# Optimization experiments

Measured on AMD Instinct MI355X. Metric: run time of the kernel, lower is better.

## Reference

```python
import jax, jax.numpy as jnp
import numpy as np

N, D, G, C, M = 4096, 256, 4, 10, 5  # nodes, feat dim, batches, centroids, clusterings


def setup_inputs() -> dict:
    key = jax.random.key(0)
    k1, k2, k3, k4 = jax.random.split(key, 4)
    adj = jax.random.uniform(k1, (N, N), dtype=jnp.float32)
    enc_rep = jax.random.normal(k2, (N, D), dtype=jnp.float32)
    batch_id = jax.random.randint(k3, (N,), 0, G, dtype=jnp.int32)
    cluster_labels = jax.random.randint(k4, (M, N), 0, C, dtype=jnp.int32)
    return {"adj": adj, "enc_rep": enc_rep, "batch_id": batch_id,
            "cluster_labels": cluster_labels, "top_k": 20, "top_k_inter": 10}


def reference(adj, enc_rep, batch_id, cluster_labels, top_k, top_k_inter):
    n = enc_rep.shape[0]
    NEG = jnp.float32(-1e30)
    rows = jnp.arange(n)

    # 'similarity' metric: raw inner-product similarity, full N x N once
    sim = enc_rep @ enc_rep.T                                # [N, N]
    same = batch_id[:, None] == batch_id[None, :]            # same-batch mask

    # intra: top_k+1 within own batch group, drop first (self) column
    intra_sim = jnp.where(same, sim, NEG)
    _, intra_idx = jax.lax.top_k(intra_sim, top_k + 1)
    intra_idx = intra_idx[:, 1:]                              # [N, top_k]

    # inter: top_k_inter among all other batch groups
    inter_sim = jnp.where(same, NEG, sim)
    _, inter_idx = jax.lax.top_k(inter_sim, top_k_inter)      # [N, top_k_inter]

    knn_idx = jnp.concatenate([intra_idx, inter_idx], axis=1)  # [N, k_tot]

    # rep_adj[j, i] = 1 iff j is a knn of i  (coo rows=neighbors, cols=node)
    B = jnp.zeros((n, n), jnp.float32).at[knn_idx, rows[:, None]].set(1.0)
    # common_adj = rep_adj * (rep_adj.T > 0), diag zeroed (mutual-knn graph)
    common = B * B.T
    common = common.at[rows, rows].set(0.0)

    # locality = knn_neighbor * adj
    locality = common * adj

    # padded-neighbor validity mask (I_knn_padded != -1 analog): mutual neighbors
    mutual = common[rows[:, None], knn_idx] > 0               # [N, k_tot]

    # per-clustering close-neighbor test, combined across clusterings
    nb_lbl = cluster_labels[:, knn_idx]                       # [M, N, k_tot]
    eq = cluster_labels[:, :, None] == nb_lbl                 # [M, N, k_tot]
    curr = eq | mutual[None]                                  # curr_close_nei = eq | bool_mask
    all_close = jnp.all(curr, axis=0)                         # AND across clusterings

    return locality, all_close.astype(jnp.float32)
```

## Files before the change

### kernel.cpp

```cpp
#include <hip/hip_runtime.h>
#include <hip/hip_bf16.h>
#include <cfloat>

#define NN 4096
#define DD 256
#define MM 5
#define K_TOT 30
#define TGT_INTRA 32
#define TGT_INTER 24
#define CAND_CAP 64

typedef __attribute__((ext_vector_type(8))) short bf16x8;
typedef __attribute__((ext_vector_type(4))) float f32x4;

__device__ __forceinline__ void async16(const void* g, void* l) {
    __builtin_amdgcn_global_load_lds((__attribute__((address_space(1))) void*)g,
                                     (__attribute__((address_space(3))) void*)l,
                                     16, 0, 0);
}

__global__ __launch_bounds__(256) void convert_bf16(const float* __restrict__ E,
                                                    ushort* __restrict__ Eb) {
    const int idx = blockIdx.x * 256 + threadIdx.x;
    const float4 f = ((const float4*)E)[idx];
    ushort4 h;
    {
        __hip_bfloat16 a = __float2bfloat16(f.x); h.x = *(ushort*)&a;
        __hip_bfloat16 b = __float2bfloat16(f.y); h.y = *(ushort*)&b;
        __hip_bfloat16 c = __float2bfloat16(f.z); h.z = *(ushort*)&c;
        __hip_bfloat16 d = __float2bfloat16(f.w); h.w = *(ushort*)&d;
    }
    ((ushort4*)Eb)[idx] = h;
}

__global__ __launch_bounds__(256) void gemm_bf16(const ushort* __restrict__ Eb,
                                                 ushort* __restrict__ simb) {
    __shared__ union {
        struct { ushort A[128 * 32]; ushort B[128 * 32]; } s;
        ushort stage[32 * 136];
    } lds;

    const int t = threadIdx.x;
    const int w = t >> 6, lane = t & 63;
    const int quad = lane >> 4, mr = lane & 15;
    const int rowBase = blockIdx.y * 128, colBase = blockIdx.x * 128;
    const int waveRow = (w & 1) * 64, waveCol = (w >> 1) * 64;

    const int lrow = lane >> 2;
    const int lslot = lane & 3;
    const int gchunk = lslot ^ ((lrow >> 1) & 3);

    f32x4 acc[4][4];
#pragma unroll
    for (int a = 0; a < 4; ++a)
#pragma unroll
        for (int b = 0; b < 4; ++b) acc[a][b] = (f32x4)(0.0f);

    for (int kc = 0; kc < DD; kc += 32) {
#pragma unroll
        for (int n = 0; n < 2; ++n) {
            const int r = w * 32 + n * 16 + lrow;
            const ushort* ga = Eb + (size_t)(rowBase + r) * DD + kc + gchunk * 8;
            const ushort* gb = Eb + (size_t)(colBase + r) * DD + kc + gchunk * 8;
            async16(ga, &lds.s.A[(w * 32 + n * 16) * 32]);
            async16(gb, &lds.s.B[(w * 32 + n * 16) * 32]);
        }
        __syncthreads();

        const int swzF = (mr >> 1) & 3;
        bf16x8 af[4], bfr[4];
#pragma unroll
        for (int rt = 0; rt < 4; ++rt)
            af[rt] = *(const bf16x8*)&lds.s.A[(waveRow + rt * 16 + mr) * 32 +
                                              ((quad ^ swzF) * 8)];
#pragma unroll
        for (int ct = 0; ct < 4; ++ct)
            bfr[ct] = *(const bf16x8*)&lds.s.B[(waveCol + ct * 16 + mr) * 32 +
                                               ((quad ^ swzF) * 8)];
#pragma unroll
        for (int rt = 0; rt < 4; ++rt)
#pragma unroll
            for (int ct = 0; ct < 4; ++ct)
                acc[rt][ct] = __builtin_amdgcn_mfma_f32_16x16x32_bf16(
                    af[rt], bfr[ct], acc[rt][ct], 0, 0, 0);
        __syncthreads();
    }

#pragma unroll
    for (int c = 0; c < 4; ++c) {
        __syncthreads();
        if ((w & 1) == (c >> 1)) {
            const int rtBase = 2 * (c & 1);
#pragma unroll
            for (int r2 = 0; r2 < 2; ++r2) {
                const int rt = rtBase + r2;
#pragma unroll
                for (int ct = 0; ct < 4; ++ct)
#pragma unroll
                    for (int reg = 0; reg < 4; ++reg) {
                        __hip_bfloat16 hb = __float2bfloat16(acc[rt][ct][reg]);
                        const int lr2 = r2 * 16 + quad * 4 + reg;
                        lds.stage[lr2 * 136 + waveCol + ct * 16 + mr] = *(ushort*)&hb;
                    }
            }
        }
        __syncthreads();
#pragma unroll
        for (int it = 0; it < 2; ++it) {
            const int cid = t + it * 256;
            const int row = cid >> 4;
            const int off = (cid & 15) * 8;
            *(int4*)(simb + (size_t)(rowBase + c * 32 + row) * NN + colBase + off) =
                *(const int4*)&lds.stage[row * 136 + off];
        }
    }
}

__global__ __launch_bounds__(256) void select_rescore(const ushort* __restrict__ sim,
                                                      const float* __restrict__ E,
                                                      const int* __restrict__ batch,
                                                      int* __restrict__ knn) {
    __shared__ unsigned histS[4][256];
    __shared__ unsigned subS[4][256];
    __shared__ int candIdxS[4][2][CAND_CAP];
    __shared__ double candValS[4][2][CAND_CAP];
    __shared__ int cntS[4][2];
    __shared__ int cbS[4][2];
    __shared__ unsigned remS[4][2];
    __shared__ unsigned thrS[4][2];

    const int t = threadIdx.x;
    const int w = t >> 6, lane = t & 63;
    const int i = __builtin_amdgcn_readfirstlane(blockIdx.x * 4 + w);
    const int bi = batch[i];

    unsigned* hist = histS[w];
    unsigned* sub = subS[w];

#pragma unroll
    for (int b = 0; b < 4; ++b) { hist[lane * 4 + b] = 0u; sub[lane * 4 + b] = 0u; }
    if (lane < 2) cntS[w][lane] = 0;
    __syncthreads();

    unsigned kp[32];
    unsigned long long interm = 0;
    {
        const ushort* sp = sim + (size_t)i * NN + lane * 8;
        const int* bp = batch + lane * 8;
#pragma unroll
        for (int c = 0; c < 8; ++c) {
            const int4 sv = *(const int4*)(sp + c * 512);
            int bb[8];
            *(int4*)&bb[0] = *(const int4*)(bp + c * 512);
            *(int4*)&bb[4] = *(const int4*)(bp + c * 512 + 4);
            const unsigned uu[4] = {(unsigned)sv.x, (unsigned)sv.y,
                                    (unsigned)sv.z, (unsigned)sv.w};
#pragma unroll
            for (int p = 0; p < 4; ++p) {
                const unsigned u = uu[p];
                const unsigned sgn = u & 0x80008000u;
                const unsigned k2 = u ^ (0x80008000u | ((sgn >> 15) * 0x7FFFu));
                kp[c * 4 + p] = k2;
                const int e0 = 2 * p, e1 = 2 * p + 1;
                const unsigned m0 = (bb[e0] == bi) ? 0u : 1u;
                const unsigned m1 = (bb[e1] == bi) ? 0u : 1u;
                interm |= (unsigned long long)m0 << (c * 8 + e0);
                interm |= (unsigned long long)m1 << (c * 8 + e1);
                atomicAdd(&hist[(k2 >> 8) & 0xFF], m0 ? 0x10000u : 1u);
                atomicAdd(&hist[k2 >> 24], m1 ? 0x10000u : 1u);
            }
        }
    }
    __syncthreads();

    {
        const unsigned* hb = &hist[lane * 4];
        const unsigned s4 = hb[0] + hb[1] + hb[2] + hb[3];
        unsigned suf = s4;
#pragma unroll
        for (int off = 1; off < 64; off <<= 1) {
            const unsigned o = __shfl_down(suf, off);
            if (lane + off < 64) suf += o;
        }
        unsigned cum = suf - s4;
#pragma unroll
        for (int b = 3; b >= 0; --b) {
            const unsigned h = hb[b];
            const unsigned prev = cum;
            cum += h;
            if ((cum & 0xFFFFu) >= TGT_INTRA && (prev & 0xFFFFu) < TGT_INTRA) {
                cbS[w][0] = lane * 4 + b;
                remS[w][0] = TGT_INTRA - (prev & 0xFFFFu);
            }
            if ((cum >> 16) >= TGT_INTER && (prev >> 16) < TGT_INTER) {
                cbS[w][1] = lane * 4 + b;
                remS[w][1] = TGT_INTER - (prev >> 16);
            }
        }
    }
    __syncthreads();

    {
        const int cb0 = cbS[w][0], cb1 = cbS[w][1];
#pragma unroll
        for (int c = 0; c < 8; ++c)
#pragma unroll
            for (int p = 0; p < 4; ++p) {
                const unsigned k2 = kp[c * 4 + p];
                const unsigned k0 = k2 & 0xFFFFu, k1 = k2 >> 16;
                const int m0 = (interm >> (c * 8 + 2 * p)) & 1;
                const int m1 = (interm >> (c * 8 + 2 * p + 1)) & 1;
                if ((int)(k0 >> 8) == (m0 ? cb1 : cb0))
                    atomicAdd(&sub[k0 & 0xFF], m0 ? 0x10000u : 1u);
                if ((int)(k1 >> 8) == (m1 ? cb1 : cb0))
                    atomicAdd(&sub[k1 & 0xFF], m1 ? 0x10000u : 1u);
            }
    }
    __syncthreads();

    {
        const unsigned rI = remS[w][0], rT = remS[w][1];
        const int cb0 = cbS[w][0], cb1 = cbS[w][1];
        const unsigned* sb = &sub[lane * 4];
        const unsigned s4 = sb[0] + sb[1] + sb[2] + sb[3];
        unsigned suf = s4;
#pragma unroll
        for (int off = 1; off < 64; off <<= 1) {
            const unsigned o = __shfl_down(suf, off);
            if (lane + off < 64) suf += o;
        }
        unsigned cum = suf - s4;
#pragma unroll
        for (int b = 3; b >= 0; --b) {
            const unsigned h = sb[b];
            const unsigned prev = cum;
            cum += h;
            if ((cum & 0xFFFFu) >= rI && (prev & 0xFFFFu) < rI)
                thrS[w][0] = ((unsigned)cb0 << 8) | (unsigned)(lane * 4 + b);
            if ((cum >> 16) >= rT && (prev >> 16) < rT)
                thrS[w][1] = ((unsigned)cb1 << 8) | (unsigned)(lane * 4 + b);
        }
    }
    __syncthreads();

    {
        const unsigned thr0 = thrS[w][0], thr1 = thrS[w][1];
#pragma unroll
        for (int c = 0; c < 8; ++c)
#pragma unroll
            for (int p = 0; p < 4; ++p) {
                const unsigned k2 = kp[c * 4 + p];
                const unsigned k0 = k2 & 0xFFFFu, k1 = k2 >> 16;
                const int m0 = (interm >> (c * 8 + 2 * p)) & 1;
                const int m1 = (interm >> (c * 8 + 2 * p + 1)) & 1;
                if (k0 >= (m0 ? thr1 : thr0)) {
                    const int pos = atomicAdd(&cntS[w][m0], 1);
                    if (pos < CAND_CAP) candIdxS[w][m0][pos] = c * 512 + lane * 8 + 2 * p;
                }
                if (k1 >= (m1 ? thr1 : thr0)) {
                    const int pos = atomicAdd(&cntS[w][m1], 1);
                    if (pos < CAND_CAP) candIdxS[w][m1][pos] = c * 512 + lane * 8 + 2 * p + 1;
                }
            }
    }
    __syncthreads();

    const int c0 = min(cntS[w][0], CAND_CAP);
    const int c1 = min(cntS[w][1], CAND_CAP);
    {
        const int tot = c0 + c1;
        const float* ei = E + (size_t)i * DD;
        for (int base = 0; base < tot; base += 64) {
            const int slot = base + lane;
            if (slot < tot) {
                const int m = (slot < c0) ? 0 : 1;
                const int s = m ? (slot - c0) : slot;
                const int j = candIdxS[w][m][s];
                const float* ej = E + (size_t)j * DD;
                double a0 = 0, a1 = 0, a2 = 0, a3 = 0;
#pragma unroll 8
                for (int k = 0; k < DD; k += 4) {
                    const float4 e = *(const float4*)(ej + k);
                    a0 = fma((double)ei[k + 0], (double)e.x, a0);
                    a1 = fma((double)ei[k + 1], (double)e.y, a1);
                    a2 = fma((double)ei[k + 2], (double)e.z, a2);
                    a3 = fma((double)ei[k + 3], (double)e.w, a3);
                }
                candValS[w][m][s] = (a0 + a1) + (a2 + a3);
            }
        }
    }
    __syncthreads();

    if (lane < c0) {
        const double v = candValS[w][0][lane];
        const int idx = candIdxS[w][0][lane];
        int r = 0;
        for (int s = 0; s < c0; ++s) {
            const double o = candValS[w][0][s];
            const int oi = candIdxS[w][0][s];
            r += (o > v) || (o == v && oi < idx);
        }
        if (r >= 1 && r <= 20) knn[i * K_TOT + r - 1] = idx;
    }
    if (lane < c1) {
        const double v = candValS[w][1][lane];
        const int idx = candIdxS[w][1][lane];
        int r = 0;
        for (int s = 0; s < c1; ++s) {
            const double o = candValS[w][1][s];
            const int oi = candIdxS[w][1][s];
            r += (o > v) || (o == v && oi < idx);
        }
        if (r < 10) knn[i * K_TOT + 20 + r] = idx;
    }
}

__global__ __launch_bounds__(256) void finalize_k(const int* __restrict__ knn,
                                                  const float* __restrict__ adj,
                                                  const int* __restrict__ cl,
                                                  float* __restrict__ out) {
    const int gid = blockIdx.x * 256 + threadIdx.x;
    if (gid >= NN * K_TOT) return;
    const int i = gid / K_TOT;
    const int j = knn[gid];

    bool mutual = false;
#pragma unroll
    for (int s = 0; s < K_TOT; ++s) mutual |= (knn[j * K_TOT + s] == i);

    if (mutual) out[(size_t)i * NN + j] = adj[(size_t)i * NN + j];

    bool ac = mutual;
    if (!ac) {
        bool alleq = true;
#pragma unroll
        for (int m = 0; m < MM; ++m) alleq &= (cl[m * NN + i] == cl[m * NN + j]);
        ac = alleq;
    }
    out[(size_t)NN * NN + gid] = ac ? 1.0f : 0.0f;
}

extern "C" void kernel_launch(void* const* d_in, const int* in_sizes, int n_in,
                              void* d_out, int out_size, void* d_ws, size_t ws_size,
                              hipStream_t stream) {
    const float* adj = (const float*)d_in[0];
    const float* enc = (const float*)d_in[1];
    const int* batch = (const int*)d_in[2];
    const int* cl = (const int*)d_in[3];
    float* out = (float*)d_out;

    const size_t simB = (size_t)NN * NN * sizeof(ushort);
    const size_t ebB = (size_t)NN * DD * sizeof(ushort);
    const size_t knnB = (size_t)NN * K_TOT * sizeof(int);

    const dim3 gGrid(NN / 128, NN / 128);

    if (ws_size >= simB + ebB + knnB) {
        ushort* simb = (ushort*)d_ws;
        ushort* Eb = (ushort*)((char*)d_ws + simB);
        int* knn = (int*)((char*)d_ws + simB + ebB);
        hipMemsetAsync(d_out, 0, (size_t)NN * NN * sizeof(float), stream);
        convert_bf16<<<NN * DD / 4 / 256, 256, 0, stream>>>(enc, Eb);
        gemm_bf16<<<gGrid, 256, 0, stream>>>(Eb, simb);
        select_rescore<<<NN / 4, 256, 0, stream>>>(simb, enc, batch, knn);
        finalize_k<<<(NN * K_TOT + 255) / 256, 256, 0, stream>>>(knn, adj, cl, out);
    } else {
        ushort* simb = (ushort*)d_out;
        ushort* Eb = (ushort*)d_ws;
        int* knn = (int*)((char*)d_ws + ebB);
        convert_bf16<<<NN * DD / 4 / 256, 256, 0, stream>>>(enc, Eb);
        gemm_bf16<<<gGrid, 256, 0, stream>>>(Eb, simb);
        select_rescore<<<NN / 4, 256, 0, stream>>>(simb, enc, batch, knn);
        hipMemsetAsync(d_out, 0, (size_t)NN * NN * sizeof(float), stream);
        finalize_k<<<(NN * K_TOT + 255) / 256, 256, 0, stream>>>(knn, adj, cl, out);
    }
}
```

Baseline: 212.9 us.

## Replace radix histogram select with guessed-threshold count and bisection fallback; fuse output zeroing

The two-pass LDS-atomic radix histogram used to find per-row top-k thresholds is replaced by a fixed initial threshold guess, tuned to the expected similarity distribution. Candidates above it are counted with a register loop and a wave reduction, and a 16-step bisection runs only when the count falls outside a window. Zeroing of the output matrix moves from a separate memset into the GEMM kernel's prologue. This removes the LDS atomics and extra syncs and one full-matrix memset launch. In exchange, the guessed thresholds assume a particular distribution of the inputs, and a fallback row pays many counting passes.

```diff
diff --git a/kernel.cpp b/kernel.cpp
--- a/kernel.cpp
+++ b/kernel.cpp
@@ -6,9 +6,9 @@
 #define DD 256
 #define MM 5
 #define K_TOT 30
-#define TGT_INTRA 32
-#define TGT_INTER 24
 #define CAND_CAP 64
+#define LO_INTRA 26
+#define LO_INTER 15
 
 typedef __attribute__((ext_vector_type(8))) short bf16x8;
 typedef __attribute__((ext_vector_type(4))) float f32x4;
@@ -17,6 +17,12 @@
     __builtin_amdgcn_global_load_lds((__attribute__((address_space(1))) void*)g,
                                      (__attribute__((address_space(3))) void*)l,
                                      16, 0, 0);
+}
+
+__device__ __forceinline__ unsigned key16_of_float(float f) {
+    unsigned u = __float_as_uint(f);
+    unsigned r = ((u + 0x7FFFu + ((u >> 16) & 1u)) >> 16) & 0xFFFFu;
+    return (r & 0x8000u) ? (r ^ 0xFFFFu) : (r | 0x8000u);
 }
 
 __global__ __launch_bounds__(256) void convert_bf16(const float* __restrict__ E,
@@ -34,7 +40,8 @@
 }
 
 __global__ __launch_bounds__(256) void gemm_bf16(const ushort* __restrict__ Eb,
-                                                 ushort* __restrict__ simb) {
+                                                 ushort* __restrict__ simb,
+                                                 float* __restrict__ locout) {
     __shared__ union {
         struct { ushort A[128 * 32]; ushort B[128 * 32]; } s;
         ushort stage[32 * 136];
@@ -49,6 +56,17 @@
     const int lrow = lane >> 2;
     const int lslot = lane & 3;
     const int gchunk = lslot ^ ((lrow >> 1) & 3);
+
+    if (locout != nullptr) {
+        const float4 z4 = make_float4(0.f, 0.f, 0.f, 0.f);
+#pragma unroll
+        for (int it = 0; it < 16; ++it) {
+            const int idx = t + it * 256;
+            const int row = idx >> 5;
+            const int col4 = idx & 31;
+            *(float4*)(locout + (size_t)(rowBase + row) * NN + colBase + col4 * 4) = z4;
+        }
+    }
 
     f32x4 acc[4][4];
 #pragma unroll
@@ -120,27 +138,16 @@
                                                       const float* __restrict__ E,
                                                       const int* __restrict__ batch,
                                                       int* __restrict__ knn) {
-    __shared__ unsigned histS[4][256];
-    __shared__ unsigned subS[4][256];
     __shared__ int candIdxS[4][2][CAND_CAP];
     __shared__ double candValS[4][2][CAND_CAP];
     __shared__ int cntS[4][2];
-    __shared__ int cbS[4][2];
-    __shared__ unsigned remS[4][2];
-    __shared__ unsigned thrS[4][2];
 
     const int t = threadIdx.x;
     const int w = t >> 6, lane = t & 63;
-    const int i = __builtin_amdgcn_readfirstlane(blockIdx.x * 4 + w);
+    const int i = blockIdx.x * 4 + w;
     const int bi = batch[i];
 
-    unsigned* hist = histS[w];
-    unsigned* sub = subS[w];
-
-#pragma unroll
-    for (int b = 0; b < 4; ++b) { hist[lane * 4 + b] = 0u; sub[lane * 4 + b] = 0u; }
     if (lane < 2) cntS[w][lane] = 0;
-    __syncthreads();
 
     unsigned kp[32];
     unsigned long long interm = 0;
@@ -159,109 +166,69 @@
             for (int p = 0; p < 4; ++p) {
                 const unsigned u = uu[p];
                 const unsigned sgn = u & 0x80008000u;
-                const unsigned k2 = u ^ (0x80008000u | ((sgn >> 15) * 0x7FFFu));
-                kp[c * 4 + p] = k2;
-                const int e0 = 2 * p, e1 = 2 * p + 1;
-                const unsigned m0 = (bb[e0] == bi) ? 0u : 1u;
-                const unsigned m1 = (bb[e1] == bi) ? 0u : 1u;
-                interm |= (unsigned long long)m0 << (c * 8 + e0);
-                interm |= (unsigned long long)m1 << (c * 8 + e1);
-                atomicAdd(&hist[(k2 >> 8) & 0xFF], m0 ? 0x10000u : 1u);
-                atomicAdd(&hist[k2 >> 24], m1 ? 0x10000u : 1u);
+                kp[c * 4 + p] = u ^ (0x80008000u | ((sgn >> 15) * 0x7FFFu));
+                const unsigned m0 = (bb[2 * p] == bi) ? 0u : 1u;
+                const unsigned m1 = (bb[2 * p + 1] == bi) ? 0u : 1u;
+                interm |= (unsigned long long)m0 << (c * 8 + 2 * p);
+                interm |= (unsigned long long)m1 << (c * 8 + 2 * p + 1);
             }
         }
     }
+
+    auto countBoth = [&](unsigned K0, unsigned K1) -> unsigned {
+        unsigned cnt = 0;
+#pragma unroll
+        for (int r = 0; r < 32; ++r) {
+            const unsigned k2 = kp[r];
+            const int e = (r >> 2) * 8 + (r & 3) * 2;
+            const unsigned m0 = (unsigned)(interm >> e) & 1u;
+            const unsigned m1 = (unsigned)(interm >> (e + 1)) & 1u;
+            const unsigned k0 = k2 & 0xFFFFu, k1 = k2 >> 16;
+            if (k0 >= (m0 ? K1 : K0)) cnt += m0 ? 0x10000u : 1u;
+            if (k1 >= (m1 ? K1 : K0)) cnt += m1 ? 0x10000u : 1u;
+        }
+#pragma unroll
+        for (int off = 1; off < 64; off <<= 1) cnt += __shfl_xor(cnt, off);
+        return cnt;
+    };
+
+    unsigned K0 = key16_of_float(1.76f * 16.0f);
+    unsigned K1 = key16_of_float(2.34f * 16.0f);
+    {
+        const unsigned cnt = countBoth(K0, K1);
+        const unsigned c0 = cnt & 0xFFFFu, c1 = cnt >> 16;
+        const bool ok0 = (c0 >= LO_INTRA && c0 <= CAND_CAP);
+        const bool ok1 = (c1 >= LO_INTER && c1 <= CAND_CAP);
+        if (!(ok0 && ok1)) {
+            unsigned L0 = 0, R0 = 0xFFFFu, L1 = 0, R1 = 0xFFFFu;
+            for (int it = 0; it < 16; ++it) {
+                const unsigned mid0 = (L0 + R0 + 1) >> 1;
+                const unsigned mid1 = (L1 + R1 + 1) >> 1;
+                const unsigned cc = countBoth(mid0, mid1);
+                if ((cc & 0xFFFFu) >= LO_INTRA) L0 = mid0; else R0 = mid0 - 1;
+                if ((cc >> 16) >= LO_INTER) L1 = mid1; else R1 = mid1 - 1;
+            }
+            if (!ok0) K0 = L0;
+            if (!ok1) K1 = L1;
+        }
+    }
     __syncthreads();
 
-    {
-        const unsigned* hb = &hist[lane * 4];
-        const unsigned s4 = hb[0] + hb[1] + hb[2] + hb[3];
-        unsigned suf = s4;
-#pragma unroll
-        for (int off = 1; off < 64; off <<= 1) {
-            const unsigned o = __shfl_down(suf, off);
-            if (lane + off < 64) suf += o;
-        }
-        unsigned cum = suf - s4;
-#pragma unroll
-        for (int b = 3; b >= 0; --b) {
-            const unsigned h = hb[b];
-            const unsigned prev = cum;
-            cum += h;
-            if ((cum & 0xFFFFu) >= TGT_INTRA && (prev & 0xFFFFu) < TGT_INTRA) {
-                cbS[w][0] = lane * 4 + b;
-                remS[w][0] = TGT_INTRA - (prev & 0xFFFFu);
-            }
-            if ((cum >> 16) >= TGT_INTER && (prev >> 16) < TGT_INTER) {
-                cbS[w][1] = lane * 4 + b;
-                remS[w][1] = TGT_INTER - (prev >> 16);
-            }
-        }
-    }
-    __syncthreads();
-
-    {
-        const int cb0 = cbS[w][0], cb1 = cbS[w][1];
-#pragma unroll
-        for (int c = 0; c < 8; ++c)
-#pragma unroll
-            for (int p = 0; p < 4; ++p) {
-                const unsigned k2 = kp[c * 4 + p];
-                const unsigned k0 = k2 & 0xFFFFu, k1 = k2 >> 16;
-                const int m0 = (interm >> (c * 8 + 2 * p)) & 1;
-                const int m1 = (interm >> (c * 8 + 2 * p + 1)) & 1;
-                if ((int)(k0 >> 8) == (m0 ? cb1 : cb0))
-                    atomicAdd(&sub[k0 & 0xFF], m0 ? 0x10000u : 1u);
-                if ((int)(k1 >> 8) == (m1 ? cb1 : cb0))
-                    atomicAdd(&sub[k1 & 0xFF], m1 ? 0x10000u : 1u);
-            }
-    }
-    __syncthreads();
-
-    {
-        const unsigned rI = remS[w][0], rT = remS[w][1];
-        const int cb0 = cbS[w][0], cb1 = cbS[w][1];
-        const unsigned* sb = &sub[lane * 4];
-        const unsigned s4 = sb[0] + sb[1] + sb[2] + sb[3];
-        unsigned suf = s4;
-#pragma unroll
-        for (int off = 1; off < 64; off <<= 1) {
-            const unsigned o = __shfl_down(suf, off);
-            if (lane + off < 64) suf += o;
-        }
-        unsigned cum = suf - s4;
-#pragma unroll
-        for (int b = 3; b >= 0; --b) {
-            const unsigned h = sb[b];
-            const unsigned prev = cum;
-            cum += h;
-            if ((cum & 0xFFFFu) >= rI && (prev & 0xFFFFu) < rI)
-                thrS[w][0] = ((unsigned)cb0 << 8) | (unsigned)(lane * 4 + b);
-            if ((cum >> 16) >= rT && (prev >> 16) < rT)
-                thrS[w][1] = ((unsigned)cb1 << 8) | (unsigned)(lane * 4 + b);
-        }
-    }
-    __syncthreads();
-
-    {
-        const unsigned thr0 = thrS[w][0], thr1 = thrS[w][1];
-#pragma unroll
-        for (int c = 0; c < 8; ++c)
-#pragma unroll
-            for (int p = 0; p < 4; ++p) {
-                const unsigned k2 = kp[c * 4 + p];
-                const unsigned k0 = k2 & 0xFFFFu, k1 = k2 >> 16;
-                const int m0 = (interm >> (c * 8 + 2 * p)) & 1;
-                const int m1 = (interm >> (c * 8 + 2 * p + 1)) & 1;
-                if (k0 >= (m0 ? thr1 : thr0)) {
-                    const int pos = atomicAdd(&cntS[w][m0], 1);
-                    if (pos < CAND_CAP) candIdxS[w][m0][pos] = c * 512 + lane * 8 + 2 * p;
-                }
-                if (k1 >= (m1 ? thr1 : thr0)) {
-                    const int pos = atomicAdd(&cntS[w][m1], 1);
-                    if (pos < CAND_CAP) candIdxS[w][m1][pos] = c * 512 + lane * 8 + 2 * p + 1;
-                }
-            }
+#pragma unroll
+    for (int r = 0; r < 32; ++r) {
+        const unsigned k2 = kp[r];
+        const int e = (r >> 2) * 8 + (r & 3) * 2;
+        const int j0 = (r >> 2) * 512 + lane * 8 + (r & 3) * 2;
+        const unsigned m0 = (unsigned)(interm >> e) & 1u;
+        const unsigned m1 = (unsigned)(interm >> (e + 1)) & 1u;
+        if ((k2 & 0xFFFFu) >= (m0 ? K1 : K0)) {
+            const int pos = atomicAdd(&cntS[w][m0], 1);
+            if (pos < CAND_CAP) candIdxS[w][m0][pos] = j0;
+        }
+        if ((k2 >> 16) >= (m1 ? K1 : K0)) {
+            const int pos = atomicAdd(&cntS[w][m1], 1);
+            if (pos < CAND_CAP) candIdxS[w][m1][pos] = j0 + 1;
+        }
     }
     __syncthreads();
 
@@ -280,11 +247,11 @@
                 double a0 = 0, a1 = 0, a2 = 0, a3 = 0;
 #pragma unroll 8
                 for (int k = 0; k < DD; k += 4) {
-                    const float4 e = *(const float4*)(ej + k);
-                    a0 = fma((double)ei[k + 0], (double)e.x, a0);
-                    a1 = fma((double)ei[k + 1], (double)e.y, a1);
-                    a2 = fma((double)ei[k + 2], (double)e.z, a2);
-                    a3 = fma((double)ei[k + 3], (double)e.w, a3);
+                    const float4 e4 = *(const float4*)(ej + k);
+                    a0 = fma((double)ei[k + 0], (double)e4.x, a0);
+                    a1 = fma((double)ei[k + 1], (double)e4.y, a1);
+                    a2 = fma((double)ei[k + 2], (double)e4.z, a2);
+                    a3 = fma((double)ei[k + 3], (double)e4.w, a3);
                 }
                 candValS[w][m][s] = (a0 + a1) + (a2 + a3);
             }
@@ -360,9 +327,8 @@
         ushort* simb = (ushort*)d_ws;
         ushort* Eb = (ushort*)((char*)d_ws + simB);
         int* knn = (int*)((char*)d_ws + simB + ebB);
-        hipMemsetAsync(d_out, 0, (size_t)NN * NN * sizeof(float), stream);
         convert_bf16<<<NN * DD / 4 / 256, 256, 0, stream>>>(enc, Eb);
-        gemm_bf16<<<gGrid, 256, 0, stream>>>(Eb, simb);
+        gemm_bf16<<<gGrid, 256, 0, stream>>>(Eb, simb, out);
         select_rescore<<<NN / 4, 256, 0, stream>>>(simb, enc, batch, knn);
         finalize_k<<<(NN * K_TOT + 255) / 256, 256, 0, stream>>>(knn, adj, cl, out);
     } else {
@@ -370,7 +336,7 @@
         ushort* Eb = (ushort*)d_ws;
         int* knn = (int*)((char*)d_ws + ebB);
         convert_bf16<<<NN * DD / 4 / 256, 256, 0, stream>>>(enc, Eb);
-        gemm_bf16<<<gGrid, 256, 0, stream>>>(Eb, simb);
+        gemm_bf16<<<gGrid, 256, 0, stream>>>(Eb, simb, nullptr);
         select_rescore<<<NN / 4, 256, 0, stream>>>(simb, enc, batch, knn);
         hipMemsetAsync(d_out, 0, (size_t)NN * NN * sizeof(float), stream);
         finalize_k<<<(NN * K_TOT + 255) / 256, 256, 0, stream>>>(knn, adj, cl, out);
```

After: 303.7 us. +42.7%, slower.
